# Kernel tuning notes

Hardware: AMD Instinct MI355X
Metric: run time of the kernel (lower is better)

Reference implementation:

```python
import jax, jax.numpy as jnp
import numpy as np

B, N, D, DFC, EMB, L = 16, 1024, 128, 128, 64, 4
NHOPS = (1, 2, 3, 4)  # tatic='cont': nhop(i) = i + 1
EDGE_P = 0.03


def _make_adj(k):
    u = jax.random.uniform(k, (B, N, N))
    a = u < EDGE_P
    a = a | jnp.transpose(a, (0, 2, 1))          # undirected
    a = a | jnp.eye(N, dtype=bool)[None]         # self loops
    return a.astype(jnp.float32)


def setup_inputs() -> dict:
    key = jax.random.key(0)
    ks = jax.random.split(key, 16)
    s = 0.05
    x = jax.random.normal(ks[0], (B, N, 2 * EMB), jnp.float32)
    adj1 = _make_adj(ks[1])
    adj2 = _make_adj(ks[2])
    valid = jnp.ones((B, N), jnp.float32)
    embede_w = jax.random.normal(ks[3], (D, 2 * EMB)) * s
    gW = jax.random.normal(ks[4], (L, D, D)) * s
    gb = jnp.zeros((L, D), jnp.float32)
    gA = jax.random.normal(ks[5], (L, D, D)) * s
    gate_w = jax.random.normal(ks[6], (L, 1, 2 * D)) * s
    gate_b = jnp.zeros((L, 1), jnp.float32)
    fc0_w = jax.random.normal(ks[7], (DFC, D)) * s
    fc0_b = jnp.zeros((DFC,), jnp.float32)
    fc1_w = jax.random.normal(ks[8], (DFC, DFC)) * s
    fc1_b = jnp.zeros((DFC,), jnp.float32)
    fc2_w = jax.random.normal(ks[9], (DFC, DFC)) * s
    fc2_b = jnp.zeros((DFC,), jnp.float32)
    fc3_w = jax.random.normal(ks[10], (1, DFC)) * s
    fc3_b = jnp.zeros((1,), jnp.float32)
    return dict(x=x, adj1=adj1, adj2=adj2, valid=valid, embede_w=embede_w,
                gW=gW, gb=gb, gA=gA, gate_w=gate_w, gate_b=gate_b,
                fc0_w=fc0_w, fc0_b=fc0_b, fc1_w=fc1_w, fc1_b=fc1_b,
                fc2_w=fc2_w, fc2_b=fc2_b, fc3_w=fc3_w, fc3_b=fc3_b)


def _glema(x, adj, W, b, A, gw, gbias, nhop):
    h = x @ W.T + b                                        # [B,N,D]
    e = jnp.einsum('bjl,bkl->bjk', jnp.einsum('bjd,de->bje', h, A), h)
    e = e + jnp.transpose(e, (0, 2, 1))                    # undirected
    att = jnp.where(adj > 0, e, jnp.float32(0.0))
    att = jax.nn.softmax(att, axis=1) * adj                # softmax over dim 1, then adj mask
    az = jax.nn.relu(jnp.einsum('bij,bjd->bid', att, h))
    coeff = jax.nn.sigmoid(jnp.concatenate([h, az], -1) @ gw.T + gbias)  # [B,N,1]
    z = h
    for _ in range(nhop):
        az = jax.nn.relu(jnp.einsum('bij,bjd->bid', att, z))
        z = coeff * h + (1.0 - coeff) * az
    return z


def reference(x, adj1, adj2, valid, embede_w, gW, gb, gA, gate_w, gate_b,
              fc0_w, fc0_b, fc1_w, fc1_b, fc2_w, fc2_b, fc3_w, fc3_b):
    h = x @ embede_w.T                                     # embede (no bias)
    for k in range(L):                                     # branch='both': c_hs2 - c_hs1
        h1 = _glema(h, adj1, gW[k], gb[k], gA[k], gate_w[k], gate_b[k], NHOPS[k])
        h2 = _glema(h, adj2, gW[k], gb[k], gA[k], gate_w[k], gate_b[k], NHOPS[k])
        h = h2 - h1                                        # dropout p used in eval mode -> identity
    h = h * valid[..., None]
    pooled = h.sum(1) / valid.sum(1, keepdims=True)        # [B,D]
    y = jax.nn.relu(pooled @ fc0_w.T + fc0_b)
    y = jax.nn.relu(y @ fc1_w.T + fc1_b)
    y = jax.nn.relu(y @ fc2_w.T + fc2_b)
    y = jax.nn.sigmoid(y @ fc3_w.T + fc3_b)
    return y.reshape(-1)                                   # [B]
```

## Files before the change

kernel.cpp:

```cpp
#include <hip/hip_runtime.h>

typedef _Float16 half_t;
typedef _Float16 half8 __attribute__((ext_vector_type(8)));
typedef float floatx4 __attribute__((ext_vector_type(4)));

#define MFMA(a,b,c) __builtin_amdgcn_mfma_f32_16x16x32_f16(a,b,c,0,0,0)

#define NB 16
#define NLEN 1024
#define DD 128
#define BN (NB*NLEN)
#define BND ((size_t)NB*NLEN*DD)
#define EMP 1044

__global__ __launch_bounds__(256)
void k_cast(const float* __restrict__ gW, const float* __restrict__ gA,
            const float* __restrict__ Ew,
            half_t* __restrict__ Wf, half_t* __restrict__ STf, half_t* __restrict__ EwF) {
    int i = blockIdx.x * 256 + threadIdx.x;
    if (i < 65536) {
        Wf[i] = (half_t)gW[i];
        int base = i & ~16383;
        int lrem = i & 16383;
        int d = lrem >> 7, e = lrem & 127;
        STf[base + (e << 7) + d] = (half_t)(gA[i] + gA[base + (e << 7) + d]);
    } else {
        int j = i - 65536;
        EwF[j] = (half_t)Ew[j];
    }
}

__global__ __launch_bounds__(256)
void k_emb(const float* __restrict__ x, const half_t* __restrict__ EwF,
           half_t* __restrict__ h16) {
    __shared__ half_t htile[32 * 136];
    __shared__ half_t otile[32 * 136];
    int g = blockIdx.x * 32;
    int t = threadIdx.x;
    int w = t >> 6, l = t & 63, q = l >> 4, l15 = l & 15;
#pragma unroll
    for (int v = 0; v < 2; v++) {
        int idx = v * 256 + t; int r = idx >> 4, c8 = (idx & 15) * 8;
        const float* xp = &x[(size_t)(g + r) * DD + c8];
        float4 f0 = *(const float4*)xp;
        float4 f1 = *(const float4*)(xp + 4);
        half8 va;
        va[0] = (half_t)f0.x; va[1] = (half_t)f0.y; va[2] = (half_t)f0.z; va[3] = (half_t)f0.w;
        va[4] = (half_t)f1.x; va[5] = (half_t)f1.y; va[6] = (half_t)f1.z; va[7] = (half_t)f1.w;
        *(half8*)&htile[r * 136 + c8] = va;
    }
    __syncthreads();
    int rowh = (w & 1) * 16;
    int c0 = (w >> 1) * 4;
    half8 a1[4];
#pragma unroll
    for (int kc = 0; kc < 4; kc++) a1[kc] = *(const half8*)&htile[(rowh + l15) * 136 + kc * 32 + q * 8];
#pragma unroll
    for (int cc = 0; cc < 4; cc++) {
        int col = (c0 + cc) * 16 + l15;
        floatx4 a = {0.f, 0.f, 0.f, 0.f};
#pragma unroll
        for (int kc = 0; kc < 4; kc++) {
            half8 bf = *(const half8*)&EwF[((size_t)col << 7) + kc * 32 + q * 8];
            a = MFMA(a1[kc], bf, a);
        }
#pragma unroll
        for (int r = 0; r < 4; r++)
            otile[(rowh + q * 4 + r) * 136 + col] = (half_t)a[r];
    }
    __syncthreads();
#pragma unroll
    for (int v = 0; v < 2; v++) {
        int idx = v * 256 + t; int r = idx >> 4, c8 = (idx & 15) * 8;
        *(half8*)&h16[((size_t)(g + r) << 7) + c8] = *(const half8*)&otile[r * 136 + c8];
    }
}

__global__ __launch_bounds__(256, 8)
void k_mask(const float* __restrict__ adj1, const float* __restrict__ adj2,
            unsigned short* __restrict__ mask16) {
    int t = threadIdx.x, w = t >> 6, l = t & 63;
    int wave = blockIdx.x * 4 + w;
    int R0 = wave * 8;
    int br = R0 >> 14, nb0 = R0 & 16383;
    const float* arow = (br ? adj2 : adj1) + (size_t)nb0 * 1024 + l * 16;
    float4 v0 = *(const float4*)&arow[0];
    float4 v1 = *(const float4*)&arow[4];
    float4 v2 = *(const float4*)&arow[8];
    float4 v3 = *(const float4*)&arow[12];
    unsigned short* mp = mask16 + (size_t)R0 * 64 + l;
#pragma unroll
    for (int it = 0; it < 8; it++) {
        float4 c0 = v0, c1 = v1, c2 = v2, c3 = v3;
        if (it < 7) {
            const float* nx = arow + (size_t)(it + 1) * 1024;
            v0 = *(const float4*)&nx[0];
            v1 = *(const float4*)&nx[4];
            v2 = *(const float4*)&nx[8];
            v3 = *(const float4*)&nx[12];
        }
        unsigned m = 0u;
        m |= (c0.x > 0.f ? 1u : 0u);        m |= (c0.y > 0.f ? 2u : 0u);
        m |= (c0.z > 0.f ? 4u : 0u);        m |= (c0.w > 0.f ? 8u : 0u);
        m |= (c1.x > 0.f ? 0x10u : 0u);     m |= (c1.y > 0.f ? 0x20u : 0u);
        m |= (c1.z > 0.f ? 0x40u : 0u);     m |= (c1.w > 0.f ? 0x80u : 0u);
        m |= (c2.x > 0.f ? 0x100u : 0u);    m |= (c2.y > 0.f ? 0x200u : 0u);
        m |= (c2.z > 0.f ? 0x400u : 0u);    m |= (c2.w > 0.f ? 0x800u : 0u);
        m |= (c3.x > 0.f ? 0x1000u : 0u);   m |= (c3.y > 0.f ? 0x2000u : 0u);
        m |= (c3.z > 0.f ? 0x4000u : 0u);   m |= (c3.w > 0.f ? 0x8000u : 0u);
        mp[it * 64] = (unsigned short)m;
    }
}

__global__ __launch_bounds__(256)
void k_proj(const half_t* __restrict__ pa, const half_t* __restrict__ pb,
            const half_t* __restrict__ Wf, const float* __restrict__ bias,
            const half_t* __restrict__ STf,
            half_t* __restrict__ hbr16, half_t* __restrict__ hbrT,
            half_t* __restrict__ hbrF, half_t* __restrict__ hSF) {
    __shared__ half_t htile[32 * 136];
    __shared__ half_t hbtile[32 * 136];
    int g = blockIdx.x * 32;
    int t = threadIdx.x;
    int w = t >> 6, l = t & 63, q = l >> 4, l15 = l & 15;
#pragma unroll
    for (int v = 0; v < 2; v++) {
        int idx = v * 256 + t; int r = idx >> 4, c8 = (idx & 15) * 8;
        half8 va = *(const half8*)&pa[((size_t)(g + r) << 7) + c8];
        if (pb) {
            half8 vb = *(const half8*)&pb[((size_t)(g + r) << 7) + c8];
            va = va - vb;
        }
        *(half8*)&htile[r * 136 + c8] = va;
    }
    __syncthreads();
    int rowh = (w & 1) * 16;
    int c0 = (w >> 1) * 4;
    half8 a1[4];
#pragma unroll
    for (int kc = 0; kc < 4; kc++) a1[kc] = *(const half8*)&htile[(rowh + l15) * 136 + kc * 32 + q * 8];
    floatx4 acc[4];
#pragma unroll
    for (int cc = 0; cc < 4; cc++) {
        int col = (c0 + cc) * 16 + l15;
        floatx4 a = {0.f, 0.f, 0.f, 0.f};
#pragma unroll
        for (int kc = 0; kc < 4; kc++) {
            half8 bf = *(const half8*)&Wf[((size_t)col << 7) + kc * 32 + q * 8];
            a = MFMA(a1[kc], bf, a);
        }
        float bv = bias[col];
        a.x += bv; a.y += bv; a.z += bv; a.w += bv;
        acc[cc] = a;
    }
#pragma unroll
    for (int cc = 0; cc < 4; cc++) {
        int col = (c0 + cc) * 16 + l15;
#pragma unroll
        for (int r = 0; r < 4; r++)
            hbtile[(rowh + q * 4 + r) * 136 + col] = (half_t)acc[cc][r];
    }
    __syncthreads();
    half8 a2[4];
#pragma unroll
    for (int kc = 0; kc < 4; kc++) a2[kc] = *(const half8*)&hbtile[(rowh + l15) * 136 + kc * 32 + q * 8];
#pragma unroll
    for (int cc = 0; cc < 4; cc++) {
        int col = (c0 + cc) * 16 + l15;
        floatx4 a = {0.f, 0.f, 0.f, 0.f};
#pragma unroll
        for (int kc = 0; kc < 4; kc++) {
            half8 bf = *(const half8*)&STf[((size_t)col << 7) + kc * 32 + q * 8];
            a = MFMA(a2[kc], bf, a);
        }
        acc[cc] = a;
    }
    __syncthreads();
#pragma unroll
    for (int cc = 0; cc < 4; cc++) {
        int col = (c0 + cc) * 16 + l15;
#pragma unroll
        for (int r = 0; r < 4; r++) htile[(rowh + q * 4 + r) * 136 + col] = (half_t)acc[cc][r];
    }
    __syncthreads();
#pragma unroll
    for (int v = 0; v < 2; v++) {
        int idx = v * 256 + t; int r = idx >> 4, c8 = (idx & 15) * 8;
        *(half8*)&hbr16[((size_t)(g + r) << 7) + c8] = *(const half8*)&hbtile[r * 136 + c8];
    }
    {
        int b_ = g >> 10, gi = g & 1023;
        int d = t >> 1, hh = t & 1;
        half8 r0, r1;
#pragma unroll
        for (int e = 0; e < 8; e++) {
            r0[e] = hbtile[(hh * 16 + e) * 136 + d];
            r1[e] = hbtile[(hh * 16 + 8 + e) * 136 + d];
        }
        half_t* op = hbrT + ((size_t)b_ * 128 + d) * 1024 + gi + hh * 16;
        *(half8*)op = r0;
        *(half8*)(op + 8) = r1;
    }
#pragma unroll
    for (int v = 0; v < 2; v++) {
        int fi = v * 256 + t;
        int g2 = fi >> 8, kc = (fi >> 6) & 3, li = fi & 63;
        int src = (g2 * 16 + (li & 15)) * 136 + kc * 32 + (li >> 4) * 8;
        size_t dst = (((size_t)(blockIdx.x * 2 + g2) * 4 + kc) << 10) + li * 8;
        *(half8*)&hbrF[dst] = *(const half8*)&hbtile[src];
        *(half8*)&hSF[dst]  = *(const half8*)&htile[src];
    }
}

__global__ __launch_bounds__(256)
void k_E(const half_t* __restrict__ hSF, const half_t* __restrict__ hbrF,
         const unsigned short* __restrict__ mask16, const half_t* __restrict__ hbrT,
         half_t* __restrict__ Dm, float* __restrict__ rsr, half_t* __restrict__ hbrsT) {
    int hw = blockIdx.y * 64 + blockIdx.x;
    int wk = (hw & 7) * 128 + (hw >> 3);
    int b = wk >> 6, s = wk & 63;
    int t = threadIdx.x, w = t >> 6, l = t & 63, q = l >> 4, l15 = l & 15;
    __shared__ half_t emS[16 * EMP];
    __shared__ float rsS[2][16];
    size_t Gb = (size_t)b * 64;
    half8 A[4];
#pragma unroll
    for (int kc = 0; kc < 4; kc++)
        A[kc] = *(const half8*)&hSF[(((Gb + s) * 4 + kc) << 10) + l * 8];
#pragma unroll 4
    for (int cg = 0; cg < 16; cg++) {
        int c0 = w * 256 + cg * 16;
        floatx4 a = {0.f, 0.f, 0.f, 0.f};
#pragma unroll
        for (int kc = 0; kc < 4; kc++) {
            half8 bf = *(const half8*)&hbrF[(((Gb + w * 16 + cg) * 4 + kc) << 10) + l * 8];
            a = MFMA(A[kc], bf, a);
        }
#pragma unroll
        for (int r = 0; r < 4; r++)
            emS[(q * 4 + r) * EMP + c0 + l15] = (half_t)a[r];
    }
    __syncthreads();
    const float CN = 0.000335462627903f;
#pragma unroll
    for (int tt = 0; tt < 8; tt++) {
        int task = tt * 4 + w;
        int rl = task >> 1, br = task & 1;
        size_t R = ((size_t)br << 14) + (size_t)b * 1024 + s * 16 + rl;
        unsigned mv = (unsigned)mask16[R * 64 + l];
        half8 e0 = *(const half8*)&emS[rl * EMP + l * 16];
        half8 e1 = *(const half8*)&emS[rl * EMP + l * 16 + 8];
        half8 o0, o1;
        float rs = 0.f;
#pragma unroll
        for (int c2 = 0; c2 < 8; c2++) {
            float v0 = ((mv >> c2) & 1u) ? __expf((float)e0[c2] - 8.f) : 0.f;
            float v1 = ((mv >> (c2 + 8)) & 1u) ? __expf((float)e1[c2] - 8.f) : 0.f;
            o0[c2] = (half_t)v0; o1[c2] = (half_t)v1;
            rs += v0 + v1;
        }
        *(half8*)&Dm[R * 1024 + l * 16] = o0;
        *(half8*)&Dm[R * 1024 + l * 16 + 8] = o1;
        int cn = __popc(mv);
        rs += __shfl_xor(rs, 1); rs += __shfl_xor(rs, 2);
        rs += __shfl_xor(rs, 4); rs += __shfl_xor(rs, 8);
        rs += __shfl_xor(rs, 16); rs += __shfl_xor(rs, 32);
        cn += __shfl_xor(cn, 1); cn += __shfl_xor(cn, 2);
        cn += __shfl_xor(cn, 4); cn += __shfl_xor(cn, 8);
        cn += __shfl_xor(cn, 16); cn += __shfl_xor(cn, 32);
        if (l == 0) {
            float rv = 1.f / (rs + (1024.f - (float)cn) * CN);
            rsr[R] = rv;
            rsS[br][rl] = rv;
        }
    }
    __syncthreads();
    {
        int d = t >> 1, br = t & 1;
        const half_t* hp = hbrT + ((size_t)b * 128 + d) * 1024 + s * 16;
        half8 a0 = *(const half8*)hp, a1 = *(const half8*)(hp + 8);
        half8 r0, r1;
#pragma unroll
        for (int e = 0; e < 8; e++) {
            r0[e] = (half_t)((float)a0[e] * rsS[br][e]);
            r1[e] = (half_t)((float)a1[e] * rsS[br][8 + e]);
        }
        half_t* op = hbrsT + (((size_t)((br << 4) + b)) * 128 + d) * 1024 + s * 16;
        *(half8*)op = r0;
        *(half8*)(op + 8) = r1;
    }
}

__global__ __launch_bounds__(512)
void k_azd(const half_t* __restrict__ Dm, const float* __restrict__ rsr,
           const half_t* __restrict__ BT, const half_t* __restrict__ hbr16,
           const float* __restrict__ gw, const float* __restrict__ gb_,
           float* __restrict__ cfb, half_t* __restrict__ outR, half_t* __restrict__ outT,
           int mode) {
    __shared__ union {
        struct { half_t A[2][128][72]; half_t B[2][128][72]; } s;
        half_t az[128][136];
    } sm;
    int t = threadIdx.x, w = t >> 6, l = t & 63, q = l >> 4, l15 = l & 15;
    int wi = w & 3, wd = w >> 2;
    int bid = blockIdx.x;
    int slice = bid & 31, tile = bid >> 5;
    int br = slice & 1, b = slice >> 1;
    int c = (br << 4) + b;
    int i0 = tile * 128;
    const half_t* Dp = Dm + ((size_t)c << 20) + (size_t)i0 * 1024;
    const half_t* Bp = BT + ((size_t)c << 17);
    int ar = t >> 3, ac = (t & 7) * 8;
    half8 ra0, ra1, rb0, rb1;
    ra0 = *(const half8*)&Dp[(size_t)ar * 1024 + ac];
    ra1 = *(const half8*)&Dp[(size_t)(ar + 64) * 1024 + ac];
    rb0 = *(const half8*)&Bp[(size_t)ar * 1024 + ac];
    rb1 = *(const half8*)&Bp[(size_t)(ar + 64) * 1024 + ac];
    *(half8*)&sm.s.A[0][ar][ac] = ra0;
    *(half8*)&sm.s.A[0][ar + 64][ac] = ra1;
    *(half8*)&sm.s.B[0][ar][ac] = rb0;
    *(half8*)&sm.s.B[0][ar + 64][ac] = rb1;
    __syncthreads();
    floatx4 acc[2][4] = {};
    for (int kt = 0; kt < 16; kt++) {
        int buf = kt & 1;
        if (kt < 15) {
            int ko = (kt + 1) * 64;
            ra0 = *(const half8*)&Dp[(size_t)ar * 1024 + ko + ac];
            ra1 = *(const half8*)&Dp[(size_t)(ar + 64) * 1024 + ko + ac];
            rb0 = *(const half8*)&Bp[(size_t)ar * 1024 + ko + ac];
            rb1 = *(const half8*)&Bp[(size_t)(ar + 64) * 1024 + ko + ac];
        }
#pragma unroll
        for (int kk = 0; kk < 2; kk++) {
            half8 af0 = *(const half8*)&sm.s.A[buf][wi * 32 + l15][kk * 32 + q * 8];
            half8 af1 = *(const half8*)&sm.s.A[buf][wi * 32 + 16 + l15][kk * 32 + q * 8];
#pragma unroll
            for (int nf = 0; nf < 4; nf++) {
                half8 bf = *(const half8*)&sm.s.B[buf][wd * 64 + nf * 16 + l15][kk * 32 + q * 8];
                acc[0][nf] = MFMA(af0, bf, acc[0][nf]);
                acc[1][nf] = MFMA(af1, bf, acc[1][nf]);
            }
        }
        __syncthreads();
        if (kt < 15) {
            int nbuf = buf ^ 1;
            *(half8*)&sm.s.A[nbuf][ar][ac] = ra0;
            *(half8*)&sm.s.A[nbuf][ar + 64][ac] = ra1;
            *(half8*)&sm.s.B[nbuf][ar][ac] = rb0;
            *(half8*)&sm.s.B[nbuf][ar + 64][ac] = rb1;
            __syncthreads();
        }
    }
#pragma unroll
    for (int sub = 0; sub < 2; sub++)
#pragma unroll
        for (int nf = 0; nf < 4; nf++)
#pragma unroll
            for (int r = 0; r < 4; r++)
                sm.az[wi * 32 + sub * 16 + q * 4 + r][wd * 64 + nf * 16 + l15] = (half_t)acc[sub][nf][r];
    __syncthreads();
#pragma unroll
    for (int it = 0; it < 4; it++) {
        int iloc = it * 32 + (t >> 4);
        int i = i0 + iloc;
        int nb = b * 1024 + i;
        int R = c * 1024 + i;
        half8 az8 = *(const half8*)&sm.az[iloc][l15 * 8];
        half8 hv8 = *(const half8*)&hbr16[((size_t)nb << 7) + l15 * 8];
        float av[8], hv[8];
#pragma unroll
        for (int d = 0; d < 8; d++) {
            av[d] = fmaxf((float)az8[d], 0.f);
            hv[d] = (float)hv8[d];
        }
        float cf;
        if (mode >= 3) {
            const float* g1 = gw + l15 * 8;
            const float* g2 = gw + 128 + l15 * 8;
            float dp = 0.f;
#pragma unroll
            for (int d = 0; d < 8; d++) dp += hv[d] * g1[d] + av[d] * g2[d];
            dp += __shfl_xor(dp, 1); dp += __shfl_xor(dp, 2);
            dp += __shfl_xor(dp, 4); dp += __shfl_xor(dp, 8);
            cf = 1.f / (1.f + __expf(-(dp + gb_[0])));
            if (l15 == 0) cfb[R] = cf;
        } else {
            cf = cfb[R];
        }
        if (mode == 2 || mode == 4) {
            half8 o;
#pragma unroll
            for (int d = 0; d < 8; d++) o[d] = (half_t)(cf * hv[d] + (1.f - cf) * av[d]);
            *(half8*)&outR[(size_t)R * DD + l15 * 8] = o;
        } else {
            float sc = rsr[R];
#pragma unroll
            for (int d = 0; d < 8; d++)
                sm.az[iloc][l15 * 8 + d] = (half_t)(sc * (cf * hv[d] + (1.f - cf) * av[d]));
        }
    }
    if (mode == 1 || mode == 3) {
        __syncthreads();
        int d = t & 127, g4 = t >> 7;
        half_t* op = outT + ((size_t)c * 128 + d) * 1024 + i0 + g4 * 32;
        half8 r0, r1, r2, r3;
#pragma unroll
        for (int e = 0; e < 8; e++) {
            r0[e] = sm.az[g4 * 32 + e][d];
            r1[e] = sm.az[g4 * 32 + 8 + e][d];
            r2[e] = sm.az[g4 * 32 + 16 + e][d];
            r3[e] = sm.az[g4 * 32 + 24 + e][d];
        }
        *(half8*)op = r0;
        *(half8*)(op + 8) = r1;
        *(half8*)(op + 16) = r2;
        *(half8*)(op + 24) = r3;
    }
}

__global__ __launch_bounds__(256)
void k_pool(const half_t* __restrict__ z2, const half_t* __restrict__ z1,
            const float* __restrict__ valid, float* __restrict__ part) {
    int b = blockIdx.y, s = blockIdx.x;
    int t = threadIdx.x, d = t & 127, hf = t >> 7;
    __shared__ float red[128];
    float acc = 0.f;
    int nbase = s * 128 + hf * 64;
    for (int n = nbase; n < nbase + 64; n++) {
        size_t gi = ((size_t)(b * 1024 + n) << 7) + d;
        acc += ((float)z2[gi] - (float)z1[gi]) * valid[b * 1024 + n];
    }
    if (hf) red[d] = acc;
    __syncthreads();
    if (!hf) part[(b * 8 + s) * 128 + d] = acc + red[d];
}

__global__ __launch_bounds__(128)
void k_mlp(const float* __restrict__ part, const float* __restrict__ valid,
           const float* __restrict__ w0, const float* __restrict__ b0,
           const float* __restrict__ w1, const float* __restrict__ b1,
           const float* __restrict__ w2, const float* __restrict__ b2,
           const float* __restrict__ w3, const float* __restrict__ b3,
           float* __restrict__ out) {
    int b = blockIdx.x, t = threadIdx.x;
    __shared__ float y0[DD], y1[DD];
    __shared__ float sred[2];
    float vs = 0.f;
    for (int n = t; n < NLEN; n += 128) vs += valid[b * NLEN + n];
    for (int off = 32; off; off >>= 1) vs += __shfl_down(vs, off);
    if ((t & 63) == 0) sred[t >> 6] = vs;
    __syncthreads();
    float vsum = sred[0] + sred[1];
    float acc = 0.f;
#pragma unroll
    for (int s = 0; s < 8; s++) acc += part[(b * 8 + s) * 128 + t];
    y0[t] = acc / vsum;
    __syncthreads();
    float a = b0[t];
    for (int k = 0; k < DD; k++) a += y0[k] * w0[t * DD + k];
    y1[t] = fmaxf(a, 0.f);
    __syncthreads();
    a = b1[t];
    for (int k = 0; k < DD; k++) a += y1[k] * w1[t * DD + k];
    y0[t] = fmaxf(a, 0.f);
    __syncthreads();
    a = b2[t];
    for (int k = 0; k < DD; k++) a += y0[k] * w2[t * DD + k];
    y1[t] = fmaxf(a, 0.f);
    __syncthreads();
    float pv = y1[t] * w3[t];
    for (int off = 32; off; off >>= 1) pv += __shfl_down(pv, off);
    if ((t & 63) == 0) sred[t >> 6] = pv;
    __syncthreads();
    if (t == 0) out[b] = 1.f / (1.f + __expf(-(sred[0] + sred[1] + b3[0])));
}

extern "C" void kernel_launch(void* const* d_in, const int* in_sizes, int n_in,
                              void* d_out, int out_size, void* d_ws, size_t ws_size,
                              hipStream_t stream) {
    (void)in_sizes; (void)n_in; (void)out_size; (void)ws_size;
    const float* x     = (const float*)d_in[0];
    const float* adj1  = (const float*)d_in[1];
    const float* adj2  = (const float*)d_in[2];
    const float* valid = (const float*)d_in[3];
    const float* Ew    = (const float*)d_in[4];
    const float* gW    = (const float*)d_in[5];
    const float* gb    = (const float*)d_in[6];
    const float* gA    = (const float*)d_in[7];
    const float* gatew = (const float*)d_in[8];
    const float* gateb = (const float*)d_in[9];
    const float* w0 = (const float*)d_in[10]; const float* b0 = (const float*)d_in[11];
    const float* w1 = (const float*)d_in[12]; const float* b1 = (const float*)d_in[13];
    const float* w2 = (const float*)d_in[14]; const float* b2 = (const float*)d_in[15];
    const float* w3 = (const float*)d_in[16]; const float* b3 = (const float*)d_in[17];
    float* out = (float*)d_out;

    char* p = (char*)d_ws;
    float* rsr  = (float*)p; p += 2 * BN * 4;
    float* cfb  = (float*)p; p += 2 * BN * 4;
    float* partb = (float*)p; p += (size_t)NB * 8 * 128 * 4;
    half_t* h16   = (half_t*)p; p += BND * 2;
    half_t* hbr16 = (half_t*)p; p += BND * 2;
    half_t* hbrF  = (half_t*)p; p += BND * 2;
    half_t* hSF   = (half_t*)p; p += BND * 2;
    half_t* hbrT  = (half_t*)p; p += BND * 2;
    half_t* hbrsT = (half_t*)p; p += 2 * BND * 2;
    half_t* zf    = (half_t*)p; p += 2 * BND * 2;
    half_t* zTA   = (half_t*)p; p += 2 * BND * 2;
    half_t* zTB   = (half_t*)p; p += 2 * BND * 2;
    unsigned short* mask16 = (unsigned short*)p; p += (size_t)2 * BN * 64 * 2;
    half_t* Dm   = (half_t*)p; p += (size_t)2 * BN * 1024 * 2;
    half_t* Wf16 = (half_t*)p; p += (size_t)4 * 128 * 128 * 2;
    half_t* ST16 = (half_t*)p; p += (size_t)4 * 128 * 128 * 2;
    half_t* EwF  = (half_t*)p; p += (size_t)128 * 128 * 2;

    k_cast<<<320, 256, 0, stream>>>(gW, gA, Ew, Wf16, ST16, EwF);
    k_emb<<<512, 256, 0, stream>>>(x, EwF, h16);
    k_mask<<<1024, 256, 0, stream>>>(adj1, adj2, mask16);

    for (int k = 0; k < 4; k++) {
        int nhop = k + 1;
        const half_t* pa = k ? (zf + BND) : h16;
        const half_t* pb = k ? zf : nullptr;
        k_proj<<<512, 256, 0, stream>>>(pa, pb, Wf16 + (size_t)k * 16384, gb + k * 128,
                                        ST16 + (size_t)k * 16384, hbr16, hbrT, hbrF, hSF);
        k_E<<<dim3(64, NB), 256, 0, stream>>>(hSF, hbrF, mask16, hbrT, Dm, rsr, hbrsT);
        if (nhop == 1) {
            k_azd<<<256, 512, 0, stream>>>(Dm, rsr, hbrsT, hbr16, gatew + k * 256, gateb + k,
                                           cfb, zf, (half_t*)nullptr, 4);
        } else {
            k_azd<<<256, 512, 0, stream>>>(Dm, rsr, hbrsT, hbr16, gatew + k * 256, gateb + k,
                                           cfb, (half_t*)nullptr, zTA, 3);
        }
        const half_t* srcT = zTA;
        for (int hop = 2; hop <= nhop; hop++) {
            if (hop == nhop) {
                k_azd<<<256, 512, 0, stream>>>(Dm, rsr, srcT, hbr16, gatew + k * 256, gateb + k,
                                               cfb, zf, (half_t*)nullptr, 2);
            } else {
                half_t* dT = (hop & 1) ? zTA : zTB;
                k_azd<<<256, 512, 0, stream>>>(Dm, rsr, srcT, hbr16, gatew + k * 256, gateb + k,
                                               cfb, (half_t*)nullptr, dT, 1);
                srcT = dT;
            }
        }
    }
    k_pool<<<dim3(8, NB), 256, 0, stream>>>(zf + BND, zf, valid, partb);
    k_mlp<<<16, 128, 0, stream>>>(partb, valid, w0, b0, w1, b1, w2, b2, w3, b3, out);
}
```

Baseline: 637.6 us.

## Fuse attention score recomputation into aggregation kernel, drop dense Dm matrix

```diff
diff --git a/kernel.cpp b/kernel.cpp
--- a/kernel.cpp
+++ b/kernel.cpp
@@ -215,7 +215,7 @@
 __global__ __launch_bounds__(256)
 void k_E(const half_t* __restrict__ hSF, const half_t* __restrict__ hbrF,
          const unsigned short* __restrict__ mask16, const half_t* __restrict__ hbrT,
-         half_t* __restrict__ Dm, float* __restrict__ rsr, half_t* __restrict__ hbrsT) {
+         float* __restrict__ rsr, half_t* __restrict__ hbrsT) {
     int hw = blockIdx.y * 64 + blockIdx.x;
     int wk = (hw & 7) * 128 + (hw >> 3);
     int b = wk >> 6, s = wk & 63;
@@ -250,17 +250,13 @@
         unsigned mv = (unsigned)mask16[R * 64 + l];
         half8 e0 = *(const half8*)&emS[rl * EMP + l * 16];
         half8 e1 = *(const half8*)&emS[rl * EMP + l * 16 + 8];
-        half8 o0, o1;
         float rs = 0.f;
 #pragma unroll
         for (int c2 = 0; c2 < 8; c2++) {
             float v0 = ((mv >> c2) & 1u) ? __expf((float)e0[c2] - 8.f) : 0.f;
             float v1 = ((mv >> (c2 + 8)) & 1u) ? __expf((float)e1[c2] - 8.f) : 0.f;
-            o0[c2] = (half_t)v0; o1[c2] = (half_t)v1;
             rs += v0 + v1;
         }
-        *(half8*)&Dm[R * 1024 + l * 16] = o0;
-        *(half8*)&Dm[R * 1024 + l * 16 + 8] = o1;
         int cn = __popc(mv);
         rs += __shfl_xor(rs, 1); rs += __shfl_xor(rs, 2);
         rs += __shfl_xor(rs, 4); rs += __shfl_xor(rs, 8);
@@ -292,73 +288,94 @@
 }
 
 __global__ __launch_bounds__(512)
-void k_azd(const half_t* __restrict__ Dm, const float* __restrict__ rsr,
+void k_azf(const half_t* __restrict__ hSF, const half_t* __restrict__ hbrF,
+           const unsigned short* __restrict__ mask16, const float* __restrict__ rsr,
            const half_t* __restrict__ BT, const half_t* __restrict__ hbr16,
            const float* __restrict__ gw, const float* __restrict__ gb_,
            float* __restrict__ cfb, half_t* __restrict__ outR, half_t* __restrict__ outT,
            int mode) {
+    __shared__ unsigned short maskL[128][64];
     __shared__ union {
-        struct { half_t A[2][128][72]; half_t B[2][128][72]; } s;
-        half_t az[128][136];
+        half_t hb[32768];
+        struct { half_t P[128 * 136]; half_t zf[16384]; } pv;
     } sm;
     int t = threadIdx.x, w = t >> 6, l = t & 63, q = l >> 4, l15 = l & 15;
-    int wi = w & 3, wd = w >> 2;
     int bid = blockIdx.x;
     int slice = bid & 31, tile = bid >> 5;
     int br = slice & 1, b = slice >> 1;
     int c = (br << 4) + b;
     int i0 = tile * 128;
-    const half_t* Dp = Dm + ((size_t)c << 20) + (size_t)i0 * 1024;
-    const half_t* Bp = BT + ((size_t)c << 17);
-    int ar = t >> 3, ac = (t & 7) * 8;
-    half8 ra0, ra1, rb0, rb1;
-    ra0 = *(const half8*)&Dp[(size_t)ar * 1024 + ac];
-    ra1 = *(const half8*)&Dp[(size_t)(ar + 64) * 1024 + ac];
-    rb0 = *(const half8*)&Bp[(size_t)ar * 1024 + ac];
-    rb1 = *(const half8*)&Bp[(size_t)(ar + 64) * 1024 + ac];
-    *(half8*)&sm.s.A[0][ar][ac] = ra0;
-    *(half8*)&sm.s.A[0][ar + 64][ac] = ra1;
-    *(half8*)&sm.s.B[0][ar][ac] = rb0;
-    *(half8*)&sm.s.B[0][ar + 64][ac] = rb1;
-    __syncthreads();
-    floatx4 acc[2][4] = {};
-    for (int kt = 0; kt < 16; kt++) {
-        int buf = kt & 1;
-        if (kt < 15) {
-            int ko = (kt + 1) * 64;
-            ra0 = *(const half8*)&Dp[(size_t)ar * 1024 + ko + ac];
-            ra1 = *(const half8*)&Dp[(size_t)(ar + 64) * 1024 + ko + ac];
-            rb0 = *(const half8*)&Bp[(size_t)ar * 1024 + ko + ac];
-            rb1 = *(const half8*)&Bp[(size_t)(ar + 64) * 1024 + ko + ac];
-        }
-#pragma unroll
-        for (int kk = 0; kk < 2; kk++) {
-            half8 af0 = *(const half8*)&sm.s.A[buf][wi * 32 + l15][kk * 32 + q * 8];
-            half8 af1 = *(const half8*)&sm.s.A[buf][wi * 32 + 16 + l15][kk * 32 + q * 8];
-#pragma unroll
-            for (int nf = 0; nf < 4; nf++) {
-                half8 bf = *(const half8*)&sm.s.B[buf][wd * 64 + nf * 16 + l15][kk * 32 + q * 8];
-                acc[0][nf] = MFMA(af0, bf, acc[0][nf]);
-                acc[1][nf] = MFMA(af1, bf, acc[1][nf]);
+    {
+        const uint4* src = (const uint4*)(mask16 + ((size_t)c * 1024 + i0) * 64);
+        uint4* dst = (uint4*)&maskL[0][0];
+        dst[t] = src[t];
+        dst[t + 512] = src[t + 512];
+    }
+    half8 As[4];
+    size_t stripg = (size_t)b * 64 + tile * 8 + w;
+#pragma unroll
+    for (int kc = 0; kc < 4; kc++)
+        As[kc] = *(const half8*)&hSF[((stripg * 4 + kc) << 10) + l * 8];
+    floatx4 accp[8] = {};
+    const half_t* zsrc = BT + ((size_t)c << 17);
+    const half_t* hbsrc = hbrF + (((size_t)b * 256) << 10);
+    __syncthreads();
+    for (int jb = 0; jb < 8; jb++) {
+        {
+            const half8* s8 = (const half8*)(hbsrc + ((size_t)jb * 32 << 10));
+            half8* d8 = (half8*)sm.hb;
+#pragma unroll
+            for (int rep = 0; rep < 8; rep++)
+                d8[rep * 512 + t] = s8[rep * 512 + t];
+        }
+        __syncthreads();
+        floatx4 as[8];
+#pragma unroll
+        for (int cg = 0; cg < 8; cg++) {
+            floatx4 a = {0.f, 0.f, 0.f, 0.f};
+#pragma unroll
+            for (int kc = 0; kc < 4; kc++) {
+                half8 bf = *(const half8*)&sm.hb[((cg * 4 + kc) << 10) + l * 8];
+                a = MFMA(As[kc], bf, a);
             }
+            as[cg] = a;
         }
         __syncthreads();
-        if (kt < 15) {
-            int nbuf = buf ^ 1;
-            *(half8*)&sm.s.A[nbuf][ar][ac] = ra0;
-            *(half8*)&sm.s.A[nbuf][ar + 64][ac] = ra1;
-            *(half8*)&sm.s.B[nbuf][ar][ac] = rb0;
-            *(half8*)&sm.s.B[nbuf][ar + 64][ac] = rb1;
-            __syncthreads();
-        }
-    }
-#pragma unroll
-    for (int sub = 0; sub < 2; sub++)
-#pragma unroll
-        for (int nf = 0; nf < 4; nf++)
-#pragma unroll
-            for (int r = 0; r < 4; r++)
-                sm.az[wi * 32 + sub * 16 + q * 4 + r][wd * 64 + nf * 16 + l15] = (half_t)acc[sub][nf][r];
+#pragma unroll
+        for (int cg = 0; cg < 8; cg++) {
+#pragma unroll
+            for (int r = 0; r < 4; r++) {
+                int il = w * 16 + q * 4 + r;
+                unsigned mv = (unsigned)maskL[il][jb * 8 + cg];
+                float v = ((mv >> l15) & 1u) ? __expf(as[cg][r] - 8.f) : 0.f;
+                sm.pv.P[il * 136 + cg * 16 + l15] = (half_t)v;
+            }
+        }
+#pragma unroll
+        for (int rep = 0; rep < 4; rep++) {
+            int chunk = rep * 512 + t;
+            int d = chunk >> 4, x = chunk & 15;
+            half8 v = *(const half8*)&zsrc[(size_t)d * 1024 + jb * 128 + x * 8];
+            int li = ((x & 3) << 4) | (d & 15);
+            *(half8*)&sm.pv.zf[(((d >> 4) * 4 + (x >> 2)) << 9) + li * 8] = v;
+        }
+        __syncthreads();
+#pragma unroll
+        for (int kc = 0; kc < 4; kc++) {
+            half8 af = *(const half8*)&sm.pv.P[(w * 16 + l15) * 136 + kc * 32 + q * 8];
+#pragma unroll
+            for (int cg = 0; cg < 8; cg++) {
+                half8 bf = *(const half8*)&sm.pv.zf[((cg * 4 + kc) << 9) + l * 8];
+                accp[cg] = MFMA(af, bf, accp[cg]);
+            }
+        }
+        __syncthreads();
+    }
+#pragma unroll
+    for (int cg = 0; cg < 8; cg++)
+#pragma unroll
+        for (int r = 0; r < 4; r++)
+            sm.pv.P[(w * 16 + q * 4 + r) * 136 + cg * 16 + l15] = (half_t)accp[cg][r];
     __syncthreads();
 #pragma unroll
     for (int it = 0; it < 4; it++) {
@@ -366,7 +383,7 @@
         int i = i0 + iloc;
         int nb = b * 1024 + i;
         int R = c * 1024 + i;
-        half8 az8 = *(const half8*)&sm.az[iloc][l15 * 8];
+        half8 az8 = *(const half8*)&sm.pv.P[iloc * 136 + l15 * 8];
         half8 hv8 = *(const half8*)&hbr16[((size_t)nb << 7) + l15 * 8];
         float av[8], hv[8];
 #pragma unroll
@@ -397,7 +414,7 @@
             float sc = rsr[R];
 #pragma unroll
             for (int d = 0; d < 8; d++)
-                sm.az[iloc][l15 * 8 + d] = (half_t)(sc * (cf * hv[d] + (1.f - cf) * av[d]));
+                sm.pv.P[iloc * 136 + l15 * 8 + d] = (half_t)(sc * (cf * hv[d] + (1.f - cf) * av[d]));
         }
     }
     if (mode == 1 || mode == 3) {
@@ -407,10 +424,10 @@
         half8 r0, r1, r2, r3;
 #pragma unroll
         for (int e = 0; e < 8; e++) {
-            r0[e] = sm.az[g4 * 32 + e][d];
-            r1[e] = sm.az[g4 * 32 + 8 + e][d];
-            r2[e] = sm.az[g4 * 32 + 16 + e][d];
-            r3[e] = sm.az[g4 * 32 + 24 + e][d];
+            r0[e] = sm.pv.P[(g4 * 32 + e) * 136 + d];
+            r1[e] = sm.pv.P[(g4 * 32 + 8 + e) * 136 + d];
+            r2[e] = sm.pv.P[(g4 * 32 + 16 + e) * 136 + d];
+            r3[e] = sm.pv.P[(g4 * 32 + 24 + e) * 136 + d];
         }
         *(half8*)op = r0;
         *(half8*)(op + 8) = r1;
@@ -510,7 +527,6 @@
     half_t* zTA   = (half_t*)p; p += 2 * BND * 2;
     half_t* zTB   = (half_t*)p; p += 2 * BND * 2;
     unsigned short* mask16 = (unsigned short*)p; p += (size_t)2 * BN * 64 * 2;
-    half_t* Dm   = (half_t*)p; p += (size_t)2 * BN * 1024 * 2;
     half_t* Wf16 = (half_t*)p; p += (size_t)4 * 128 * 128 * 2;
     half_t* ST16 = (half_t*)p; p += (size_t)4 * 128 * 128 * 2;
     half_t* EwF  = (half_t*)p; p += (size_t)128 * 128 * 2;
@@ -525,23 +541,27 @@
         const half_t* pb = k ? zf : nullptr;
         k_proj<<<512, 256, 0, stream>>>(pa, pb, Wf16 + (size_t)k * 16384, gb + k * 128,
                                         ST16 + (size_t)k * 16384, hbr16, hbrT, hbrF, hSF);
-        k_E<<<dim3(64, NB), 256, 0, stream>>>(hSF, hbrF, mask16, hbrT, Dm, rsr, hbrsT);
+        k_E<<<dim3(64, NB), 256, 0, stream>>>(hSF, hbrF, mask16, hbrT, rsr, hbrsT);
         if (nhop == 1) {
-            k_azd<<<256, 512, 0, stream>>>(Dm, rsr, hbrsT, hbr16, gatew + k * 256, gateb + k,
-                                           cfb, zf, (half_t*)nullptr, 4);
+            k_azf<<<256, 512, 0, stream>>>(hSF, hbrF, mask16, rsr, hbrsT, hbr16,
+                                           gatew + k * 256, gateb + k, cfb,
+                                           zf, (half_t*)nullptr, 4);
         } else {
-            k_azd<<<256, 512, 0, stream>>>(Dm, rsr, hbrsT, hbr16, gatew + k * 256, gateb + k,
-                                           cfb, (half_t*)nullptr, zTA, 3);
+            k_azf<<<256, 512, 0, stream>>>(hSF, hbrF, mask16, rsr, hbrsT, hbr16,
+                                           gatew + k * 256, gateb + k, cfb,
+                                           (half_t*)nullptr, zTA, 3);
         }
         const half_t* srcT = zTA;
         for (int hop = 2; hop <= nhop; hop++) {
             if (hop == nhop) {
-                k_azd<<<256, 512, 0, stream>>>(Dm, rsr, srcT, hbr16, gatew + k * 256, gateb + k,
-                                               cfb, zf, (half_t*)nullptr, 2);
+                k_azf<<<256, 512, 0, stream>>>(hSF, hbrF, mask16, rsr, srcT, hbr16,
+                                               gatew + k * 256, gateb + k, cfb,
+                                               zf, (half_t*)nullptr, 2);
             } else {
                 half_t* dT = (hop & 1) ? zTA : zTB;
-                k_azd<<<256, 512, 0, stream>>>(Dm, rsr, srcT, hbr16, gatew + k * 256, gateb + k,
-                                               cfb, (half_t*)nullptr, dT, 1);
+                k_azf<<<256, 512, 0, stream>>>(hSF, hbrF, mask16, rsr, srcT, hbr16,
+                                               gatew + k * 256, gateb + k, cfb,
+                                               (half_t*)nullptr, dT, 1);
                 srcT = dT;
             }
         }
```

After: 801.5 us. +25.7%, slower.
